# Kernel tuning notes

Hardware: AMD Instinct MI355X
Metric: run time of the kernel (lower is better)

The kernel has to match this reference:

```python
import jax, jax.numpy as jnp
import numpy as np

NGRAM = 16
SUB = 512  # bytes per sub-block


def byte2image(block, ngram=NGRAM):
    """block: (B, L) int -> (B, 1, ngram*8, L-ngram) float32 in [-1, 1]."""
    B, L = block.shape
    blk = block.astype(jnp.int32)
    # nxt[:, i] = blk[:, i+1], last column zero
    nxt = jnp.concatenate([blk[:, 1:], jnp.zeros((B, 1), jnp.int32)], axis=1)
    # 8 bit-shifted views of the byte stream
    shifts = jnp.stack(
        [((blk << s) & 255) + ((nxt >> (8 - s)) & 255) for s in range(8)],
        axis=1,
    )  # (B, 8, L)
    flat = shifts.reshape(B, -1)  # (B, 8*L)
    parts = [flat] + [jnp.roll(flat, -i, axis=1) for i in range(1, ngram)]
    stacked = jnp.concatenate(parts, axis=1).reshape(B, ngram * 8, L)
    result = stacked[:, :, :-ngram].astype(jnp.float32)
    result = (result / 255.0 - 0.5) / 0.5
    return result[:, None]  # (B, 1, ngram*8, L-ngram)


def byte2image_4k(block, ngram=NGRAM):
    """block: (B, 4096) -> (B, 8, ngram*8, 512-ngram)."""
    return jnp.concatenate(
        [byte2image(block[:, i * SUB:(i + 1) * SUB], ngram) for i in range(8)],
        axis=1,
    )


def setup_inputs() -> dict:
    key = jax.random.key(0)
    kx, kw = jax.random.split(key)
    x = jax.random.randint(kx, (256, 4096), 0, 256, dtype=jnp.int64)
    W = jax.random.normal(kw, (496, 64), dtype=jnp.float32) * 0.02
    return {"x": x, "W": W}


def reference(x, W):
    # ByteFormerWrapper.forward with block_size=4096: byte2image_4k then the
    # (opaque) model; model stood in by a linear head over the image width.
    img = byte2image_4k(x)                      # (B, 8, 128, 496)
    out = jnp.einsum('bchw,wo->bcho', img, W)   # (B, 8, 128, 64)
    return out
```

## Files before the change

### kernel.cpp

```cpp
#include <hip/hip_runtime.h>

typedef unsigned short u16;
typedef unsigned int u32;
typedef _Float16 half8 __attribute__((ext_vector_type(8)));
typedef __attribute__((ext_vector_type(4))) float floatx4;

#define LSTRIDE 72
#define TILE (128 * LSTRIDE)

__global__ __launch_bounds__(256, 4) void byteformer_fused(
    const int* __restrict__ x, const float* __restrict__ Wm,
    float* __restrict__ out) {
  __shared__ __align__(16) u16 arena[2 * TILE];
  __shared__ float part[256];
  __shared__ float csumsh[64];
  u16* As = arena;
  u16* Bs = arena + TILE;

  const int t = threadIdx.x;
  const int mtile = blockIdx.x;
  const int y = blockIdx.y;

  const int wave = t >> 6, lane = t & 63;
  const int wm = wave >> 1, wn = wave & 1;
  const int quad = lane >> 4, l16 = lane & 15;

  const int sA_sub = t >> 4;
  const int sA_kg  = (t >> 1) & 7;
  const int sA_qh  = t & 1;
  const long xrow = ((long)mtile * 16 + sA_sub) * 512;

  floatx4 acc[4][4];
  #pragma unroll
  for (int mt = 0; mt < 4; ++mt)
    #pragma unroll
    for (int nt = 0; nt < 4; ++nt)
      acc[mt][nt] = floatx4{0.f, 0.f, 0.f, 0.f};

  float csum_local = 0.0f;

  int4 ca, cb; int cc;
  float fv[17];
  u32 hp[9];

  auto xload = [&](int kc) {
    const int base = kc * 64 + sA_kg * 8;
    ca = *(const int4*)&x[xrow + base];
    cb = *(const int4*)&x[xrow + base + 4];
    cc = (base + 8 < 512) ? x[xrow + base + 8] : 0;
  };

  auto wissueA = [&](int kc) {
    const int cbase = kc * 64 + 16 * wave - 2 * y - 1;
    #pragma unroll
    for (int j = 0; j < 9; ++j) {
      const int c = cbase + j;
      fv[j] = (c >= 0 && c < 496) ? Wm[c * 64 + lane] : 0.0f;
    }
  };
  auto wissueB = [&](int kc) {
    const int cbase = kc * 64 + 16 * wave - 2 * y - 1;
    #pragma unroll
    for (int j = 9; j < 17; ++j) {
      const int c = cbase + j;
      fv[j] = (c >= 0 && c < 496) ? Wm[c * 64 + lane] : 0.0f;
    }
  };
  auto wfinishA = [&]() {
    #pragma unroll
    for (int j = 1; j <= 8; ++j) csum_local += fv[j];
    #pragma unroll
    for (int i = 0; i < 4; ++i) {
      u32 h0 = __builtin_bit_cast(unsigned short, (_Float16)fv[2 * i]);
      u32 h1 = __builtin_bit_cast(unsigned short, (_Float16)fv[2 * i + 1]);
      hp[i] = h0 | (h1 << 16);
    }
  };
  auto wfinishB = [&]() {
    #pragma unroll
    for (int j = 9; j <= 16; ++j) csum_local += fv[j];
    #pragma unroll
    for (int i = 4; i < 8; ++i) {
      u32 h0 = __builtin_bit_cast(unsigned short, (_Float16)fv[2 * i]);
      u32 h1 = __builtin_bit_cast(unsigned short, (_Float16)fv[2 * i + 1]);
      hp[i] = h0 | (h1 << 16);
    }
    hp[8] = (u32)__builtin_bit_cast(unsigned short, (_Float16)fv[16]);
  };

  auto astage = [&]() {
    const u32 c0 = (u32)ca.x, c1 = (u32)ca.y, c2 = (u32)ca.z, c3 = (u32)ca.w;
    const u32 c4 = (u32)cb.x, c5 = (u32)cb.y, c6 = (u32)cb.z, c7 = (u32)cb.w;
    const u32 c8 = (u32)cc;
    const u32 P0 = ((c0 << 8) | c1) | (((c1 << 8) | c2) << 16);
    const u32 P1 = ((c2 << 8) | c3) | (((c3 << 8) | c4) << 16);
    const u32 P2 = ((c4 << 8) | c5) | (((c5 << 8) | c6) << 16);
    const u32 P3 = ((c6 << 8) | c7) | (((c7 << 8) | c8) << 16);
    u16* arow = &As[(sA_sub * 8 + sA_qh * 4) * LSTRIDE + sA_kg * 8];
    #pragma unroll
    for (int qi = 0; qi < 4; ++qi) {
      const int sh = 8 - (sA_qh * 4 + qi);
      int4 d;
      d.x = (int)(((P0 >> sh) & 0x00FF00FFu) | 0x64006400u);
      d.y = (int)(((P1 >> sh) & 0x00FF00FFu) | 0x64006400u);
      d.z = (int)(((P2 >> sh) & 0x00FF00FFu) | 0x64006400u);
      d.w = (int)(((P3 >> sh) & 0x00FF00FFu) | 0x64006400u);
      *(int4*)(arow + qi * LSTRIDE) = d;
    }
  };

  auto bstage = [&]() {
    #pragma unroll
    for (int g = 0; g < 2; ++g) {
      const int mgrp = 2 * wave + g;
      int4 d1;
      d1.x = (int)hp[4 * g + 0];
      d1.y = (int)hp[4 * g + 1];
      d1.z = (int)hp[4 * g + 2];
      d1.w = (int)hp[4 * g + 3];
      *(int4*)&Bs[(64 + lane) * LSTRIDE + mgrp * 8] = d1;
      int4 d0;
      d0.x = (int)((hp[4 * g + 0] >> 16) | (hp[4 * g + 1] << 16));
      d0.y = (int)((hp[4 * g + 1] >> 16) | (hp[4 * g + 2] << 16));
      d0.z = (int)((hp[4 * g + 2] >> 16) | (hp[4 * g + 3] << 16));
      d0.w = (int)((hp[4 * g + 3] >> 16) | (hp[4 * g + 4] << 16));
      *(int4*)&Bs[lane * LSTRIDE + mgrp * 8] = d0;
    }
  };

  auto compute_ks = [&](int ks) {
    const int koff = ks * 32 + quad * 8;
    half8 bf[4];
    #pragma unroll
    for (int nt = 0; nt < 4; ++nt)
      bf[nt] = *(const half8*)&Bs[(wn * 64 + nt * 16 + l16) * LSTRIDE + koff];
    #pragma unroll
    for (int mt = 0; mt < 4; ++mt) {
      half8 af = *(const half8*)&As[(wm * 64 + mt * 16 + l16) * LSTRIDE + koff];
      #pragma unroll
      for (int nt = 0; nt < 4; ++nt)
        acc[mt][nt] = __builtin_amdgcn_mfma_f32_16x16x32_f16(
            af, bf[nt], acc[mt][nt], 0, 0, 0);
    }
  };

  xload(0);
  wissueA(0); wissueB(0);
  wfinishA(); wfinishB();

  for (int kc = 0; kc < 8; ++kc) {
    __syncthreads();
    astage();
    bstage();
    __syncthreads();
    if (kc < 7) { xload(kc + 1); wissueA(kc + 1); }
    compute_ks(0);
    if (kc < 7) { wfinishA(); wissueB(kc + 1); }
    compute_ks(1);
    if (kc < 7) { wfinishB(); }
  }

  const float S = 2.0f / 255.0f;
  const float K1 = 1024.0f * S + 1.0f;
  part[t] = csum_local;
  __syncthreads();
  if (t < 64)
    csumsh[t] = K1 * (part[t] + part[t + 64] + part[t + 128] + part[t + 192]);
  __syncthreads();

  float cs[4];
  #pragma unroll
  for (int nt = 0; nt < 4; ++nt) cs[nt] = csumsh[nt * 16 + l16];

  float* ep = (float*)arena;
  #pragma unroll
  for (int h = 0; h < 2; ++h) {
    if (wm == h) {
      #pragma unroll
      for (int mt = 0; mt < 4; ++mt)
        #pragma unroll
        for (int i = 0; i < 4; ++i) {
          const int mr = mt * 16 + quad * 4 + i;
          const int rowbase = (mr >> 3) * 1040 + wn * 512 + (mr & 7) * 64 + l16;
          #pragma unroll
          for (int nt = 0; nt < 4; ++nt)
            ep[rowbase + nt * 16] = __builtin_fmaf(S, acc[mt][nt][i], -cs[nt]);
        }
    }
    __syncthreads();
    const long outb =
        ((long)mtile * 16 + (long)h * 8) * 8192 + (long)y * 1024;
    #pragma unroll
    for (int k2 = 0; k2 < 8; ++k2) {
      const float4 v =
          *(const float4*)((const char*)ep + k2 * 4160 + wave * 1024 + lane * 16);
      *(float4*)&out[outb + (long)k2 * 8192 + wave * 256 + lane * 4] = v;
    }
    if (h == 0) __syncthreads();
  }
}

extern "C" void kernel_launch(void* const* d_in, const int* in_sizes, int n_in,
                              void* d_out, int out_size, void* d_ws, size_t ws_size,
                              hipStream_t stream) {
  const int* x = (const int*)d_in[0];
  const float* Wm = (const float*)d_in[1];
  float* out = (float*)d_out;
  byteformer_fused<<<dim3(128, 8), dim3(256), 0, stream>>>(x, Wm, out);
}
```

Baseline: 118.1 us.

## XOR-swizzle LDS tiles and simplify weight prefetch into single load stage

Applies an XOR swizzle to the 16-byte chunk index when writing and reading the A and B LDS tiles, to cut bank conflicts on the MFMA operand reads. It also merges the split weight-issue and finish steps into one prefetch of all 17 weight rows at the top of each iteration, with conversion and column-sum work moved into the B staging step. The loop is restructured so staging for the next chunk happens after compute. This drops the interleaving of global loads with MFMA work, which may expose more load latency or raise register pressure.

```diff
diff --git a/kernel.cpp b/kernel.cpp
--- a/kernel.cpp
+++ b/kernel.cpp
@@ -41,7 +41,6 @@
 
   int4 ca, cb; int cc;
   float fv[17];
-  u32 hp[9];
 
   auto xload = [&](int kc) {
     const int base = kc * 64 + sA_kg * 8;
@@ -50,42 +49,13 @@
     cc = (base + 8 < 512) ? x[xrow + base + 8] : 0;
   };
 
-  auto wissueA = [&](int kc) {
+  auto wload = [&](int kc) {
     const int cbase = kc * 64 + 16 * wave - 2 * y - 1;
     #pragma unroll
-    for (int j = 0; j < 9; ++j) {
+    for (int j = 0; j < 17; ++j) {
       const int c = cbase + j;
       fv[j] = (c >= 0 && c < 496) ? Wm[c * 64 + lane] : 0.0f;
     }
-  };
-  auto wissueB = [&](int kc) {
-    const int cbase = kc * 64 + 16 * wave - 2 * y - 1;
-    #pragma unroll
-    for (int j = 9; j < 17; ++j) {
-      const int c = cbase + j;
-      fv[j] = (c >= 0 && c < 496) ? Wm[c * 64 + lane] : 0.0f;
-    }
-  };
-  auto wfinishA = [&]() {
-    #pragma unroll
-    for (int j = 1; j <= 8; ++j) csum_local += fv[j];
-    #pragma unroll
-    for (int i = 0; i < 4; ++i) {
-      u32 h0 = __builtin_bit_cast(unsigned short, (_Float16)fv[2 * i]);
-      u32 h1 = __builtin_bit_cast(unsigned short, (_Float16)fv[2 * i + 1]);
-      hp[i] = h0 | (h1 << 16);
-    }
-  };
-  auto wfinishB = [&]() {
-    #pragma unroll
-    for (int j = 9; j <= 16; ++j) csum_local += fv[j];
-    #pragma unroll
-    for (int i = 4; i < 8; ++i) {
-      u32 h0 = __builtin_bit_cast(unsigned short, (_Float16)fv[2 * i]);
-      u32 h1 = __builtin_bit_cast(unsigned short, (_Float16)fv[2 * i + 1]);
-      hp[i] = h0 | (h1 << 16);
-    }
-    hp[8] = (u32)__builtin_bit_cast(unsigned short, (_Float16)fv[16]);
   };
 
   auto astage = [&]() {
@@ -96,7 +66,8 @@
     const u32 P1 = ((c2 << 8) | c3) | (((c3 << 8) | c4) << 16);
     const u32 P2 = ((c4 << 8) | c5) | (((c5 << 8) | c6) << 16);
     const u32 P3 = ((c6 << 8) | c7) | (((c7 << 8) | c8) << 16);
-    u16* arow = &As[(sA_sub * 8 + sA_qh * 4) * LSTRIDE + sA_kg * 8];
+    u16* arow = &As[(sA_sub * 8 + sA_qh * 4) * LSTRIDE +
+                    ((sA_kg ^ (sA_sub & 7)) << 3)];
     #pragma unroll
     for (int qi = 0; qi < 4; ++qi) {
       const int sh = 8 - (sA_qh * 4 + qi);
@@ -111,32 +82,48 @@
 
   auto bstage = [&]() {
     #pragma unroll
+    for (int j = 1; j <= 16; ++j) csum_local += fv[j];
+    u32 hp[9];
+    #pragma unroll
+    for (int i = 0; i < 8; ++i) {
+      u32 h0 = __builtin_bit_cast(unsigned short, (_Float16)fv[2 * i]);
+      u32 h1 = __builtin_bit_cast(unsigned short, (_Float16)fv[2 * i + 1]);
+      hp[i] = h0 | (h1 << 16);
+    }
+    hp[8] = (u32)__builtin_bit_cast(unsigned short, (_Float16)fv[16]);
+    const int physc = lane >> 3;
+    #pragma unroll
     for (int g = 0; g < 2; ++g) {
       const int mgrp = 2 * wave + g;
+      const int ch = (mgrp ^ physc) << 3;
       int4 d1;
       d1.x = (int)hp[4 * g + 0];
       d1.y = (int)hp[4 * g + 1];
       d1.z = (int)hp[4 * g + 2];
       d1.w = (int)hp[4 * g + 3];
-      *(int4*)&Bs[(64 + lane) * LSTRIDE + mgrp * 8] = d1;
+      *(int4*)&Bs[(64 + lane) * LSTRIDE + ch] = d1;
       int4 d0;
       d0.x = (int)((hp[4 * g + 0] >> 16) | (hp[4 * g + 1] << 16));
       d0.y = (int)((hp[4 * g + 1] >> 16) | (hp[4 * g + 2] << 16));
       d0.z = (int)((hp[4 * g + 2] >> 16) | (hp[4 * g + 3] << 16));
       d0.w = (int)((hp[4 * g + 3] >> 16) | (hp[4 * g + 4] << 16));
-      *(int4*)&Bs[lane * LSTRIDE + mgrp * 8] = d0;
+      *(int4*)&Bs[lane * LSTRIDE + ch] = d0;
     }
   };
 
   auto compute_ks = [&](int ks) {
-    const int koff = ks * 32 + quad * 8;
     half8 bf[4];
     #pragma unroll
-    for (int nt = 0; nt < 4; ++nt)
-      bf[nt] = *(const half8*)&Bs[(wn * 64 + nt * 16 + l16) * LSTRIDE + koff];
+    for (int nt = 0; nt < 4; ++nt) {
+      const int row = wn * 64 + nt * 16 + l16;
+      const int ch = ((ks * 4 + quad) ^ ((row >> 3) & 7)) << 3;
+      bf[nt] = *(const half8*)&Bs[row * LSTRIDE + ch];
+    }
     #pragma unroll
     for (int mt = 0; mt < 4; ++mt) {
-      half8 af = *(const half8*)&As[(wm * 64 + mt * 16 + l16) * LSTRIDE + koff];
+      const int row = wm * 64 + mt * 16 + l16;
+      const int ch = ((ks * 4 + quad) ^ ((row >> 3) & 7)) << 3;
+      half8 af = *(const half8*)&As[row * LSTRIDE + ch];
       #pragma unroll
       for (int nt = 0; nt < 4; ++nt)
         acc[mt][nt] = __builtin_amdgcn_mfma_f32_16x16x32_f16(
@@ -144,20 +131,20 @@
     }
   };
 
-  xload(0);
-  wissueA(0); wissueB(0);
-  wfinishA(); wfinishB();
+  xload(0); wload(0);
+  astage(); bstage();
+  __syncthreads();
 
   for (int kc = 0; kc < 8; ++kc) {
-    __syncthreads();
-    astage();
-    bstage();
-    __syncthreads();
-    if (kc < 7) { xload(kc + 1); wissueA(kc + 1); }
+    if (kc < 7) { xload(kc + 1); wload(kc + 1); }
     compute_ks(0);
-    if (kc < 7) { wfinishA(); wissueB(kc + 1); }
     compute_ks(1);
-    if (kc < 7) { wfinishB(); }
+    if (kc < 7) {
+      __syncthreads();
+      astage();
+      bstage();
+      __syncthreads();
+    }
   }
 
   const float S = 2.0f / 255.0f;
```

New measurement: 124.6 us. 1.06x slower.
